# Kernel optimization log

Measured on AMD Instinct MI355X. Metric: run time of the kernel, lower is better.

The kernel has to match this reference:

```python
import jax, jax.numpy as jnp
import numpy as np

B, T, D = 256, 1024, 64          # batch, timesteps, num motor units (input_dim)
H, IC_DIM, F_DIM = 128, 100, 3   # hidden_dim, IC_dim, factors_dim


def setup_inputs() -> dict:
    key = jax.random.key(0)
    ks = jax.random.split(key, 16)
    s = 0.08  # ~1/sqrt(H) scale like torch default init
    f32 = jnp.float32
    return {
        "mu_batch": jax.random.normal(ks[0], (B, T, D), f32),
        # Encoder GRU (input D -> hidden H), PyTorch gate order [r, z, n]
        "We_ih": jax.random.normal(ks[1], (3 * H, D), f32) * s,
        "We_hh": jax.random.normal(ks[2], (3 * H, H), f32) * s,
        "be_ih": jax.random.normal(ks[3], (3 * H,), f32) * s,
        "be_hh": jax.random.normal(ks[4], (3 * H,), f32) * s,
        # IC layer H -> IC_DIM
        "W_ic": jax.random.normal(ks[5], (IC_DIM, H), f32) * s,
        "b_ic": jax.random.normal(ks[6], (IC_DIM,), f32) * s,
        # Generator GRU (input IC_DIM -> hidden H)
        "Wg_ih": jax.random.normal(ks[7], (3 * H, IC_DIM), f32) * s,
        "Wg_hh": jax.random.normal(ks[8], (3 * H, H), f32) * s,
        "bg_ih": jax.random.normal(ks[9], (3 * H,), f32) * s,
        "bg_hh": jax.random.normal(ks[10], (3 * H,), f32) * s,
        # GenToFactors H -> F_DIM
        "W_gf": jax.random.normal(ks[11], (F_DIM, H), f32) * s,
        "b_gf": jax.random.normal(ks[12], (F_DIM,), f32) * s,
        # FactorsToRates F_DIM -> D
        "W_fr": jax.random.normal(ks[13], (D, F_DIM), f32) * s,
        "b_fr": jax.random.normal(ks[14], (D,), f32) * s,
    }


def _gru_step(W_hh, b_hh):
    """PyTorch GRU cell: x_proj = W_ih @ x + b_ih precomputed, gate order r,z,n."""
    def step(h, x_proj):
        gh = h @ W_hh.T + b_hh
        xr, xz, xn = jnp.split(x_proj, 3, axis=-1)
        hr, hz, hn = jnp.split(gh, 3, axis=-1)
        r = jax.nn.sigmoid(xr + hr)
        z = jax.nn.sigmoid(xz + hz)
        n = jnp.tanh(xn + r * hn)
        h_new = (1.0 - z) * n + z * h
        return h_new, h_new
    return step


def reference(mu_batch, We_ih, We_hh, be_ih, be_hh, W_ic, b_ic,
              Wg_ih, Wg_hh, bg_ih, bg_hh, W_gf, b_gf, W_fr, b_fr):
    Bsz, Tlen, _ = mu_batch.shape
    Hdim = We_hh.shape[1]
    h0 = jnp.zeros((Bsz, Hdim), mu_batch.dtype)

    # ----- Encoder GRU: only final hidden state is used -----
    x_proj = jnp.einsum('btd,gd->btg', mu_batch, We_ih) + be_ih   # [B,T,3H]
    h_enc, _ = jax.lax.scan(_gru_step(We_hh, be_hh), h0,
                            jnp.swapaxes(x_proj, 0, 1))           # [B,H]

    # ----- IC layer -----
    IC = h_enc @ W_ic.T + b_ic                                    # [B,IC]

    # ----- Generator GRU: constant input IC fed for T steps, init hidden = h_enc -----
    ic_proj = IC @ Wg_ih.T + bg_ih                                # [B,3H], constant per step
    gstep = _gru_step(Wg_hh, bg_hh)
    def gen_step(h, _):
        return gstep(h, ic_proj)
    _, gen_out = jax.lax.scan(gen_step, h_enc, None, length=Tlen) # [T,B,H]
    gen_out = jnp.swapaxes(gen_out, 0, 1)                         # [B,T,H] == full_gen_out

    # ----- Readout -----
    factors = jnp.einsum('bth,fh->btf', gen_out, W_gf) + b_gf     # [B,T,F]
    rates = jnp.einsum('btf,df->btd', jnp.exp(factors), W_fr) + b_fr  # [B,T,D]
    return rates
```

## Files before the change

### kernel.cpp

```cpp
#include <hip/hip_runtime.h>
#include <hip/hip_bf16.h>

#define Bn 256
#define Tn 1024
#define Dn 64
#define Hn 128
#define G3 384
#define ICn 100
#define BT 16
#define NTH 512
#define LDH 136
#define LDX 72

typedef _Float16 f16;
typedef __attribute__((ext_vector_type(8))) _Float16 f16x8;
typedef __attribute__((ext_vector_type(4))) _Float16 f16x4;
typedef __attribute__((ext_vector_type(4))) float f32x4;

#define MFMA(a, b, c) __builtin_amdgcn_mfma_f32_16x16x32_f16((a), (b), (c), 0, 0, 0)

__device__ __forceinline__ float rcpa(float x) { return __builtin_amdgcn_rcpf(x); }
__device__ __forceinline__ float sigm(float x) { return rcpa(1.0f + __expf(-x)); }
__device__ __forceinline__ float tanha(float x) {
    float t = __expf(-2.0f * x);
    return fmaf(2.0f, rcpa(1.0f + t), -1.0f);
}

__device__ __forceinline__ f16x8 ldw(const float* W, int row, int ldk, int k0) {
    const float* p = W + (size_t)row * ldk + k0;
    f16x8 r;
#pragma unroll
    for (int j = 0; j < 8; ++j) r[j] = (f16)p[j];
    return r;
}

__global__ __launch_bounds__(NTH, 2)
void enc_kernel(const float* __restrict__ mu,
                const float* __restrict__ We_ih, const float* __restrict__ We_hh,
                const float* __restrict__ be_ih, const float* __restrict__ be_hh,
                float* __restrict__ h_enc)
{
    const int b0 = blockIdx.x * BT;
    const int tid = threadIdx.x;
    const int w = tid >> 6, l = tid & 63, c = l & 15, q = l >> 4;

    __shared__ f16 hbuf[2][BT * LDH];
    __shared__ f16 xstg[2][8][BT * LDX];

    const int gr = w * 16 + c, gz = Hn + w * 16 + c, gn = 2 * Hn + w * 16 + c;

    f16x8 whf[3][4], wxf[3][2];
#pragma unroll
    for (int kt = 0; kt < 4; ++kt) {
        whf[0][kt] = ldw(We_hh, gr, Hn, kt * 32 + q * 8);
        whf[1][kt] = ldw(We_hh, gz, Hn, kt * 32 + q * 8);
        whf[2][kt] = ldw(We_hh, gn, Hn, kt * 32 + q * 8);
    }
#pragma unroll
    for (int kt = 0; kt < 2; ++kt) {
        wxf[0][kt] = ldw(We_ih, gr, Dn, kt * 32 + q * 8);
        wxf[1][kt] = ldw(We_ih, gz, Dn, kt * 32 + q * 8);
        wxf[2][kt] = ldw(We_ih, gn, Dn, kt * 32 + q * 8);
    }
    const float brc = be_ih[gr] + be_hh[gr];
    const float bzc = be_ih[gz] + be_hh[gz];
    const float bxn = be_ih[gn];
    const float bhn = be_hh[gn];

    float hreg[4];
#pragma unroll
    for (int r4 = 0; r4 < 4; ++r4) hreg[r4] = 0.0f;
    for (int i = tid; i < BT * Hn; i += NTH) hbuf[0][(i >> 7) * LDH + (i & 127)] = (f16)0.0f;

    const int SIT = (BT * 8 * Dn) / (NTH * 4);
#pragma unroll
    for (int i = 0; i < SIT; ++i) {
        int f = (i * NTH + tid) * 4;
        int t_off = f >> 10, rem = f & 1023;
        int bb = rem >> 6, d = rem & 63;
        const float4 v = *reinterpret_cast<const float4*>(
            mu + ((size_t)(b0 + bb) * Tn + t_off) * Dn + d);
        f16x4 h4; h4[0] = (f16)v.x; h4[1] = (f16)v.y; h4[2] = (f16)v.z; h4[3] = (f16)v.w;
        *reinterpret_cast<f16x4*>(&xstg[0][t_off][bb * LDX + d]) = h4;
    }
    __syncthreads();

    float4 pre[SIT];
    for (int t = 0; t < Tn; ++t) {
        const int ch = t >> 3, s = t & 7, cur = t & 1, sb = ch & 1;
        if (s == 0 && ch + 1 < Tn / 8) {
#pragma unroll
            for (int i = 0; i < SIT; ++i) {
                int f = (i * NTH + tid) * 4;
                int t_off = f >> 10, rem = f & 1023;
                int bb = rem >> 6, d = rem & 63;
                pre[i] = *reinterpret_cast<const float4*>(
                    mu + ((size_t)(b0 + bb) * Tn + (ch + 1) * 8 + t_off) * Dn + d);
            }
        }
        f16x8 ah[4], ax[2];
#pragma unroll
        for (int kt = 0; kt < 4; ++kt)
            ah[kt] = *reinterpret_cast<const f16x8*>(&hbuf[cur][c * LDH + kt * 32 + q * 8]);
#pragma unroll
        for (int kt = 0; kt < 2; ++kt)
            ax[kt] = *reinterpret_cast<const f16x8*>(&xstg[sb][s][c * LDX + kt * 32 + q * 8]);

        f32x4 acc0 = (f32x4){0,0,0,0}, acc1 = (f32x4){0,0,0,0};
        f32x4 acc2 = (f32x4){0,0,0,0}, accx = (f32x4){0,0,0,0};
#pragma unroll
        for (int kt = 0; kt < 4; ++kt) {
            acc0 = MFMA(ah[kt], whf[0][kt], acc0);
            acc1 = MFMA(ah[kt], whf[1][kt], acc1);
            acc2 = MFMA(ah[kt], whf[2][kt], acc2);
        }
#pragma unroll
        for (int kt = 0; kt < 2; ++kt) {
            acc0 = MFMA(ax[kt], wxf[0][kt], acc0);
            acc1 = MFMA(ax[kt], wxf[1][kt], acc1);
            accx = MFMA(ax[kt], wxf[2][kt], accx);
        }
#pragma unroll
        for (int r4 = 0; r4 < 4; ++r4) {
            float rg = sigm(acc0[r4] + brc);
            float zg = sigm(acc1[r4] + bzc);
            float hn = acc2[r4] + bhn;
            float xn = accx[r4] + bxn;
            float ng = tanha(fmaf(rg, hn, xn));
            float hv = fmaf(zg, hreg[r4] - ng, ng);
            hreg[r4] = hv;
            hbuf[cur ^ 1][(q * 4 + r4) * LDH + w * 16 + c] = (f16)hv;
        }
        if (s == 7 && ch + 1 < Tn / 8) {
#pragma unroll
            for (int i = 0; i < SIT; ++i) {
                int f = (i * NTH + tid) * 4;
                int t_off = f >> 10, rem = f & 1023;
                int bb = rem >> 6, d = rem & 63;
                f16x4 h4;
                h4[0] = (f16)pre[i].x; h4[1] = (f16)pre[i].y;
                h4[2] = (f16)pre[i].z; h4[3] = (f16)pre[i].w;
                *reinterpret_cast<f16x4*>(&xstg[sb ^ 1][t_off][bb * LDX + d]) = h4;
            }
        }
        __syncthreads();
    }
#pragma unroll
    for (int r4 = 0; r4 < 4; ++r4)
        h_enc[(size_t)(b0 + q * 4 + r4) * Hn + w * 16 + c] = hreg[r4];
}

__global__ __launch_bounds__(NTH, 2)
void gen_kernel(const float* __restrict__ h_enc,
                const float* __restrict__ W_ic, const float* __restrict__ b_ic,
                const float* __restrict__ Wg_ih, const float* __restrict__ Wg_hh,
                const float* __restrict__ bg_ih, const float* __restrict__ bg_hh,
                const float* __restrict__ W_gf, const float* __restrict__ b_gf,
                const float* __restrict__ W_fr, const float* __restrict__ b_fr,
                float* __restrict__ out)
{
    const int b0 = blockIdx.x * BT;
    const int tid = threadIdx.x;
    const int w = tid >> 6, l = tid & 63, c = l & 15, q = l >> 4;

    __shared__ f16 hbuf[2][BT * LDH];
    __shared__ float hencs[BT][Hn];
    __shared__ float ics[BT][ICn];
    __shared__ float xpcs[BT][G3];
    __shared__ float fred[2][BT][4];

    for (int i = tid; i < BT * Hn; i += NTH)
        hencs[i >> 7][i & 127] = h_enc[(size_t)(b0 + (i >> 7)) * Hn + (i & 127)];
    __syncthreads();

    for (int i = tid; i < BT * ICn; i += NTH) {
        int bb = i / ICn, j = i - bb * ICn;
        float a = b_ic[j];
        const float* wr = W_ic + (size_t)j * Hn;
#pragma unroll 4
        for (int k = 0; k < Hn; ++k) a = fmaf(wr[k], hencs[bb][k], a);
        ics[bb][j] = a;
    }
    __syncthreads();

    for (int i = tid; i < BT * G3; i += NTH) {
        int g = i >> 4, bb = i & 15;
        float a = bg_ih[g];
        const float* wr = Wg_ih + (size_t)g * ICn;
#pragma unroll 4
        for (int k = 0; k < ICn; ++k) a = fmaf(wr[k], ics[bb][k], a);
        xpcs[bb][g] = a;
    }
    for (int i = tid; i < BT * Hn; i += NTH)
        hbuf[0][(i >> 7) * LDH + (i & 127)] = (f16)hencs[i >> 7][i & 127];

    const int gr = w * 16 + c, gz = Hn + w * 16 + c, gn = 2 * Hn + w * 16 + c;

    f16x8 whf[3][4];
#pragma unroll
    for (int kt = 0; kt < 4; ++kt) {
        whf[0][kt] = ldw(Wg_hh, gr, Hn, kt * 32 + q * 8);
        whf[1][kt] = ldw(Wg_hh, gz, Hn, kt * 32 + q * 8);
        whf[2][kt] = ldw(Wg_hh, gn, Hn, kt * 32 + q * 8);
    }
    f16x8 wgff[4];
    if (w == 0) {
#pragma unroll
        for (int kt = 0; kt < 4; ++kt) {
            if (c < 3) wgff[kt] = ldw(W_gf, c, Hn, kt * 32 + q * 8);
            else {
                f16x8 z;
#pragma unroll
                for (int j = 0; j < 8; ++j) z[j] = (f16)0.0f;
                wgff[kt] = z;
            }
        }
    }
    const float bgfc = (w == 0 && c < 3) ? b_gf[c] : 0.0f;
    const int d = l;
    const float wfr0 = W_fr[d * 3 + 0], wfr1 = W_fr[d * 3 + 1], wfr2 = W_fr[d * 3 + 2];
    const float bfrd = b_fr[d];

    float hreg[4];
#pragma unroll
    for (int r4 = 0; r4 < 4; ++r4) hreg[r4] = hencs[q * 4 + r4][w * 16 + c];

    __syncthreads();

    const float bgr = bg_hh[gr], bgz = bg_hh[gz], bhn = bg_hh[gn];
    float xrc[4], xzc[4], xnc[4];
#pragma unroll
    for (int r4 = 0; r4 < 4; ++r4) {
        int bb = q * 4 + r4;
        xrc[r4] = xpcs[bb][gr] + bgr;
        xzc[r4] = xpcs[bb][gz] + bgz;
        xnc[r4] = xpcs[bb][gn];
    }

    for (int t = 0; t < Tn; ++t) {
        const int cur = t & 1;
        f16x8 ah[4];
#pragma unroll
        for (int kt = 0; kt < 4; ++kt)
            ah[kt] = *reinterpret_cast<const f16x8*>(&hbuf[cur][c * LDH + kt * 32 + q * 8]);

        f32x4 acc0 = (f32x4){0,0,0,0}, acc1 = (f32x4){0,0,0,0}, acc2 = (f32x4){0,0,0,0};
#pragma unroll
        for (int kt = 0; kt < 4; ++kt) {
            acc0 = MFMA(ah[kt], whf[0][kt], acc0);
            acc1 = MFMA(ah[kt], whf[1][kt], acc1);
            acc2 = MFMA(ah[kt], whf[2][kt], acc2);
        }
        f32x4 facc = (f32x4){0, 0, 0, 0};
        if (w == 0) {
#pragma unroll
            for (int kt = 0; kt < 4; ++kt) facc = MFMA(ah[kt], wgff[kt], facc);
        }
#pragma unroll
        for (int r4 = 0; r4 < 4; ++r4) {
            float rg = sigm(acc0[r4] + xrc[r4]);
            float zg = sigm(acc1[r4] + xzc[r4]);
            float hn = acc2[r4] + bhn;
            float ng = tanha(fmaf(rg, hn, xnc[r4]));
            float hv = fmaf(zg, hreg[r4] - ng, ng);
            hreg[r4] = hv;
            hbuf[cur ^ 1][(q * 4 + r4) * LDH + w * 16 + c] = (f16)hv;
        }
        if (w == 0 && c < 3) {
#pragma unroll
            for (int r4 = 0; r4 < 4; ++r4)
                fred[cur][q * 4 + r4][c] = __expf(facc[r4] + bgfc);
        }
        __syncthreads();
        if (t >= 1) {
            const int tout = t - 1;
#pragma unroll
            for (int rb = 0; rb < 2; ++rb) {
                int bb = w + rb * 8;
                float e0 = fred[cur][bb][0], e1 = fred[cur][bb][1], e2 = fred[cur][bb][2];
                float rate = bfrd + e0 * wfr0 + e1 * wfr1 + e2 * wfr2;
                out[((size_t)(b0 + bb) * Tn + tout) * Dn + d] = rate;
            }
        }
    }
    if (w == 0) {
        f16x8 ah[4];
#pragma unroll
        for (int kt = 0; kt < 4; ++kt)
            ah[kt] = *reinterpret_cast<const f16x8*>(&hbuf[0][c * LDH + kt * 32 + q * 8]);
        f32x4 facc = (f32x4){0, 0, 0, 0};
#pragma unroll
        for (int kt = 0; kt < 4; ++kt) facc = MFMA(ah[kt], wgff[kt], facc);
        if (c < 3) {
#pragma unroll
            for (int r4 = 0; r4 < 4; ++r4)
                fred[0][q * 4 + r4][c] = __expf(facc[r4] + bgfc);
        }
    }
    __syncthreads();
    {
#pragma unroll
        for (int rb = 0; rb < 2; ++rb) {
            int bb = w + rb * 8;
            float e0 = fred[0][bb][0], e1 = fred[0][bb][1], e2 = fred[0][bb][2];
            float rate = bfrd + e0 * wfr0 + e1 * wfr1 + e2 * wfr2;
            out[((size_t)(b0 + bb) * Tn + (Tn - 1)) * Dn + d] = rate;
        }
    }
}

extern "C" void kernel_launch(void* const* d_in, const int* in_sizes, int n_in,
                              void* d_out, int out_size, void* d_ws, size_t ws_size,
                              hipStream_t stream) {
    const float* mu    = (const float*)d_in[0];
    const float* We_ih = (const float*)d_in[1];
    const float* We_hh = (const float*)d_in[2];
    const float* be_ih = (const float*)d_in[3];
    const float* be_hh = (const float*)d_in[4];
    const float* W_ic  = (const float*)d_in[5];
    const float* b_ic  = (const float*)d_in[6];
    const float* Wg_ih = (const float*)d_in[7];
    const float* Wg_hh = (const float*)d_in[8];
    const float* bg_ih = (const float*)d_in[9];
    const float* bg_hh = (const float*)d_in[10];
    const float* W_gf  = (const float*)d_in[11];
    const float* b_gf  = (const float*)d_in[12];
    const float* W_fr  = (const float*)d_in[13];
    const float* b_fr  = (const float*)d_in[14];

    float* h_enc = (float*)d_ws;
    float* out = (float*)d_out;

    enc_kernel<<<dim3(Bn / BT), dim3(NTH), 0, stream>>>(mu, We_ih, We_hh, be_ih, be_hh, h_enc);
    gen_kernel<<<dim3(Bn / BT), dim3(NTH), 0, stream>>>(h_enc, W_ic, b_ic, Wg_ih, Wg_hh,
                                                        bg_ih, bg_hh, W_gf, b_gf, W_fr, b_fr, out);
}
```

Measured before the change: 1.613 ms.

## Fold exp2 scaling into weights and batch readout stores every eight steps

Pre-scales GRU weights and biases by -log2(e) and -2·log2(e) (and the factor weights by log2(e)), so gate activations use a raw exp2 without an extra multiply. In the generator, the factor projection rotates across warps by timestep into an 8-slot, double-parity buffer, and the output rates are written in bursts of eight rows every eighth step instead of every step. The loop is also unrolled by two with fixed read/write buffers. This cuts per-step work on the serial critical path and balances the factor work across warps, at the cost of more shared memory and burstier global stores.

```diff
diff --git a/kernel.cpp b/kernel.cpp
--- a/kernel.cpp
+++ b/kernel.cpp
@@ -19,18 +19,26 @@
 
 #define MFMA(a, b, c) __builtin_amdgcn_mfma_f32_16x16x32_f16((a), (b), (c), 0, 0, 0)
 
+#define S_SIG  (-1.4426950408889634f)
+#define S_TANH (-2.8853900817779268f)
+#define S_EXP  ( 1.4426950408889634f)
+
 __device__ __forceinline__ float rcpa(float x) { return __builtin_amdgcn_rcpf(x); }
-__device__ __forceinline__ float sigm(float x) { return rcpa(1.0f + __expf(-x)); }
-__device__ __forceinline__ float tanha(float x) {
-    float t = __expf(-2.0f * x);
-    return fmaf(2.0f, rcpa(1.0f + t), -1.0f);
-}
-
-__device__ __forceinline__ f16x8 ldw(const float* W, int row, int ldk, int k0) {
+__device__ __forceinline__ float ex2(float x) {
+#if __has_builtin(__builtin_amdgcn_exp2f)
+    return __builtin_amdgcn_exp2f(x);
+#else
+    return exp2f(x);
+#endif
+}
+__device__ __forceinline__ float sigm2(float x) { return rcpa(1.0f + ex2(x)); }
+__device__ __forceinline__ float tanh2(float x) { return fmaf(2.0f, rcpa(1.0f + ex2(x)), -1.0f); }
+
+__device__ __forceinline__ f16x8 ldw(const float* W, int row, int ldk, int k0, float s) {
     const float* p = W + (size_t)row * ldk + k0;
     f16x8 r;
 #pragma unroll
-    for (int j = 0; j < 8; ++j) r[j] = (f16)p[j];
+    for (int j = 0; j < 8; ++j) r[j] = (f16)(p[j] * s);
     return r;
 }
 
@@ -52,20 +60,20 @@
     f16x8 whf[3][4], wxf[3][2];
 #pragma unroll
     for (int kt = 0; kt < 4; ++kt) {
-        whf[0][kt] = ldw(We_hh, gr, Hn, kt * 32 + q * 8);
-        whf[1][kt] = ldw(We_hh, gz, Hn, kt * 32 + q * 8);
-        whf[2][kt] = ldw(We_hh, gn, Hn, kt * 32 + q * 8);
+        whf[0][kt] = ldw(We_hh, gr, Hn, kt * 32 + q * 8, S_SIG);
+        whf[1][kt] = ldw(We_hh, gz, Hn, kt * 32 + q * 8, S_SIG);
+        whf[2][kt] = ldw(We_hh, gn, Hn, kt * 32 + q * 8, S_TANH);
     }
 #pragma unroll
     for (int kt = 0; kt < 2; ++kt) {
-        wxf[0][kt] = ldw(We_ih, gr, Dn, kt * 32 + q * 8);
-        wxf[1][kt] = ldw(We_ih, gz, Dn, kt * 32 + q * 8);
-        wxf[2][kt] = ldw(We_ih, gn, Dn, kt * 32 + q * 8);
-    }
-    const float brc = be_ih[gr] + be_hh[gr];
-    const float bzc = be_ih[gz] + be_hh[gz];
-    const float bxn = be_ih[gn];
-    const float bhn = be_hh[gn];
+        wxf[0][kt] = ldw(We_ih, gr, Dn, kt * 32 + q * 8, S_SIG);
+        wxf[1][kt] = ldw(We_ih, gz, Dn, kt * 32 + q * 8, S_SIG);
+        wxf[2][kt] = ldw(We_ih, gn, Dn, kt * 32 + q * 8, S_TANH);
+    }
+    const float brc = S_SIG * (be_ih[gr] + be_hh[gr]);
+    const float bzc = S_SIG * (be_ih[gz] + be_hh[gz]);
+    const float bxn = S_TANH * be_ih[gn];
+    const float bhn = S_TANH * be_hh[gn];
 
     float hreg[4];
 #pragma unroll
@@ -122,11 +130,11 @@
         }
 #pragma unroll
         for (int r4 = 0; r4 < 4; ++r4) {
-            float rg = sigm(acc0[r4] + brc);
-            float zg = sigm(acc1[r4] + bzc);
+            float rg = sigm2(acc0[r4] + brc);
+            float zg = sigm2(acc1[r4] + bzc);
             float hn = acc2[r4] + bhn;
             float xn = accx[r4] + bxn;
-            float ng = tanha(fmaf(rg, hn, xn));
+            float ng = tanh2(fmaf(rg, hn, xn));
             float hv = fmaf(zg, hreg[r4] - ng, ng);
             hreg[r4] = hv;
             hbuf[cur ^ 1][(q * 4 + r4) * LDH + w * 16 + c] = (f16)hv;
@@ -167,7 +175,7 @@
     __shared__ float hencs[BT][Hn];
     __shared__ float ics[BT][ICn];
     __shared__ float xpcs[BT][G3];
-    __shared__ float fred[2][BT][4];
+    __shared__ float fredB[2][8][BT][4];
 
     for (int i = tid; i < BT * Hn; i += NTH)
         hencs[i >> 7][i & 127] = h_enc[(size_t)(b0 + (i >> 7)) * Hn + (i & 127)];
@@ -199,27 +207,27 @@
     f16x8 whf[3][4];
 #pragma unroll
     for (int kt = 0; kt < 4; ++kt) {
-        whf[0][kt] = ldw(Wg_hh, gr, Hn, kt * 32 + q * 8);
-        whf[1][kt] = ldw(Wg_hh, gz, Hn, kt * 32 + q * 8);
-        whf[2][kt] = ldw(Wg_hh, gn, Hn, kt * 32 + q * 8);
+        whf[0][kt] = ldw(Wg_hh, gr, Hn, kt * 32 + q * 8, S_SIG);
+        whf[1][kt] = ldw(Wg_hh, gz, Hn, kt * 32 + q * 8, S_SIG);
+        whf[2][kt] = ldw(Wg_hh, gn, Hn, kt * 32 + q * 8, S_TANH);
     }
     f16x8 wgff[4];
-    if (w == 0) {
-#pragma unroll
-        for (int kt = 0; kt < 4; ++kt) {
-            if (c < 3) wgff[kt] = ldw(W_gf, c, Hn, kt * 32 + q * 8);
-            else {
-                f16x8 z;
-#pragma unroll
-                for (int j = 0; j < 8; ++j) z[j] = (f16)0.0f;
-                wgff[kt] = z;
-            }
-        }
-    }
-    const float bgfc = (w == 0 && c < 3) ? b_gf[c] : 0.0f;
+#pragma unroll
+    for (int kt = 0; kt < 4; ++kt) {
+        if (c < 3) wgff[kt] = ldw(W_gf, c, Hn, kt * 32 + q * 8, S_EXP);
+        else {
+            f16x8 z;
+#pragma unroll
+            for (int j = 0; j < 8; ++j) z[j] = (f16)0.0f;
+            wgff[kt] = z;
+        }
+    }
+    const float bgfc = (c < 3) ? S_EXP * b_gf[c] : 0.0f;
     const int d = l;
     const float wfr0 = W_fr[d * 3 + 0], wfr1 = W_fr[d * 3 + 1], wfr2 = W_fr[d * 3 + 2];
     const float bfrd = b_fr[d];
+    float* op0 = out + ((size_t)(b0 + w) * Tn) * Dn + d;
+    float* op1 = out + ((size_t)(b0 + w + 8) * Tn) * Dn + d;
 
     float hreg[4];
 #pragma unroll
@@ -227,22 +235,23 @@
 
     __syncthreads();
 
-    const float bgr = bg_hh[gr], bgz = bg_hh[gz], bhn = bg_hh[gn];
+    const float bgr = bg_hh[gr], bgz = bg_hh[gz], bhnr = bg_hh[gn];
     float xrc[4], xzc[4], xnc[4];
 #pragma unroll
     for (int r4 = 0; r4 < 4; ++r4) {
         int bb = q * 4 + r4;
-        xrc[r4] = xpcs[bb][gr] + bgr;
-        xzc[r4] = xpcs[bb][gz] + bgz;
-        xnc[r4] = xpcs[bb][gn];
-    }
-
-    for (int t = 0; t < Tn; ++t) {
-        const int cur = t & 1;
+        xrc[r4] = S_SIG * (xpcs[bb][gr] + bgr);
+        xzc[r4] = S_SIG * (xpcs[bb][gz] + bgz);
+        xnc[r4] = S_TANH * xpcs[bb][gn];
+    }
+    const float bhn = S_TANH * bhnr;
+
+    auto step = [&](int t, const f16* hb_r, f16* hb_w) {
+        const int slot = t & 7, par = (t >> 3) & 1;
         f16x8 ah[4];
 #pragma unroll
         for (int kt = 0; kt < 4; ++kt)
-            ah[kt] = *reinterpret_cast<const f16x8*>(&hbuf[cur][c * LDH + kt * 32 + q * 8]);
+            ah[kt] = *reinterpret_cast<const f16x8*>(&hb_r[c * LDH + kt * 32 + q * 8]);
 
         f32x4 acc0 = (f32x4){0,0,0,0}, acc1 = (f32x4){0,0,0,0}, acc2 = (f32x4){0,0,0,0};
 #pragma unroll
@@ -251,37 +260,45 @@
             acc1 = MFMA(ah[kt], whf[1][kt], acc1);
             acc2 = MFMA(ah[kt], whf[2][kt], acc2);
         }
-        f32x4 facc = (f32x4){0, 0, 0, 0};
-        if (w == 0) {
+        if (w == slot) {
+            f32x4 facc = (f32x4){0, 0, 0, 0};
 #pragma unroll
             for (int kt = 0; kt < 4; ++kt) facc = MFMA(ah[kt], wgff[kt], facc);
+            if (c < 3) {
+#pragma unroll
+                for (int r4 = 0; r4 < 4; ++r4)
+                    fredB[par][slot][q * 4 + r4][c] = ex2(facc[r4] + bgfc);
+            }
         }
 #pragma unroll
         for (int r4 = 0; r4 < 4; ++r4) {
-            float rg = sigm(acc0[r4] + xrc[r4]);
-            float zg = sigm(acc1[r4] + xzc[r4]);
+            float rg = sigm2(acc0[r4] + xrc[r4]);
+            float zg = sigm2(acc1[r4] + xzc[r4]);
             float hn = acc2[r4] + bhn;
-            float ng = tanha(fmaf(rg, hn, xnc[r4]));
+            float ng = tanh2(fmaf(rg, hn, xnc[r4]));
             float hv = fmaf(zg, hreg[r4] - ng, ng);
             hreg[r4] = hv;
-            hbuf[cur ^ 1][(q * 4 + r4) * LDH + w * 16 + c] = (f16)hv;
-        }
-        if (w == 0 && c < 3) {
-#pragma unroll
-            for (int r4 = 0; r4 < 4; ++r4)
-                fred[cur][q * 4 + r4][c] = __expf(facc[r4] + bgfc);
+            hb_w[(q * 4 + r4) * LDH + w * 16 + c] = (f16)hv;
         }
         __syncthreads();
-        if (t >= 1) {
-            const int tout = t - 1;
-#pragma unroll
-            for (int rb = 0; rb < 2; ++rb) {
-                int bb = w + rb * 8;
-                float e0 = fred[cur][bb][0], e1 = fred[cur][bb][1], e2 = fred[cur][bb][2];
-                float rate = bfrd + e0 * wfr0 + e1 * wfr1 + e2 * wfr2;
-                out[((size_t)(b0 + bb) * Tn + tout) * Dn + d] = rate;
+        if (slot == 7) {
+            const int base_row = (t >> 3) * 8 - 1;
+#pragma unroll
+            for (int s = 0; s < 8; ++s) {
+                const int r = base_row + s;
+                if (r >= 0) {
+                    const float4 f0 = *reinterpret_cast<const float4*>(&fredB[par][s][w][0]);
+                    op0[(size_t)r * Dn] = bfrd + f0.x * wfr0 + f0.y * wfr1 + f0.z * wfr2;
+                    const float4 f1 = *reinterpret_cast<const float4*>(&fredB[par][s][w + 8][0]);
+                    op1[(size_t)r * Dn] = bfrd + f1.x * wfr0 + f1.y * wfr1 + f1.z * wfr2;
+                }
             }
         }
+    };
+
+    for (int tt = 0; tt < Tn; tt += 2) {
+        step(tt,     hbuf[0], hbuf[1]);
+        step(tt + 1, hbuf[1], hbuf[0]);
     }
     if (w == 0) {
         f16x8 ah[4];
@@ -294,18 +311,16 @@
         if (c < 3) {
 #pragma unroll
             for (int r4 = 0; r4 < 4; ++r4)
-                fred[0][q * 4 + r4][c] = __expf(facc[r4] + bgfc);
+                fredB[0][0][q * 4 + r4][c] = ex2(facc[r4] + bgfc);
         }
     }
     __syncthreads();
     {
-#pragma unroll
-        for (int rb = 0; rb < 2; ++rb) {
-            int bb = w + rb * 8;
-            float e0 = fred[0][bb][0], e1 = fred[0][bb][1], e2 = fred[0][bb][2];
-            float rate = bfrd + e0 * wfr0 + e1 * wfr1 + e2 * wfr2;
-            out[((size_t)(b0 + bb) * Tn + (Tn - 1)) * Dn + d] = rate;
-        }
+        const size_t ofs = (size_t)(Tn - 1) * Dn;
+        const float4 f0 = *reinterpret_cast<const float4*>(&fredB[0][0][w][0]);
+        op0[ofs] = bfrd + f0.x * wfr0 + f0.y * wfr1 + f0.z * wfr2;
+        const float4 f1 = *reinterpret_cast<const float4*>(&fredB[0][0][w + 8][0]);
+        op1[ofs] = bfrd + f1.x * wfr0 + f1.y * wfr1 + f1.z * wfr2;
     }
 }
 
```

New measurement: 1.509 ms. -6.4%, faster.
